# Performance work log

Hardware: AMD Instinct MI355X
Metric: run time of the kernel (lower is better)

The kernel has to match this reference:

```python
import jax, jax.numpy as jnp
import numpy as np

D_MODEL = 1024
N_HEADS = 16
N_KV = N_HEADS // 2
HEAD_DIM = D_MODEL // N_HEADS
HIDDEN = 4 * D_MODEL
B, T = 4, 2048


def setup_inputs() -> dict:
    key = jax.random.key(0)
    ks = jax.random.split(key, 10)
    s = 0.02
    return {
        "x": jax.random.normal(ks[0], (B, T, D_MODEL), dtype=jnp.float32),
        "g1": jnp.ones((D_MODEL,), jnp.float32),
        "g2": jnp.ones((D_MODEL,), jnp.float32),
        "wq": jax.random.normal(ks[1], (D_MODEL, D_MODEL), jnp.float32) * s,
        "wk": jax.random.normal(ks[2], (D_MODEL, N_KV * HEAD_DIM), jnp.float32) * s,
        "wv": jax.random.normal(ks[3], (D_MODEL, N_KV * HEAD_DIM), jnp.float32) * s,
        "wo": jax.random.normal(ks[4], (D_MODEL, D_MODEL), jnp.float32) * s,
        "w1": jax.random.normal(ks[5], (D_MODEL, HIDDEN), jnp.float32) * s,
        "w2": jax.random.normal(ks[6], (D_MODEL, HIDDEN), jnp.float32) * s,
        "w3": jax.random.normal(ks[7], (HIDDEN, D_MODEL), jnp.float32) * s,
    }


def _rmsnorm(x, g, eps=1e-6):
    return x * jax.lax.rsqrt(jnp.mean(x * x, axis=-1, keepdims=True) + eps) * g


def _rope(q, k):
    # q: [B,H,T,d], k: [B,Hkv,T,d]; half-split rotary as in the torch RoPE
    d = q.shape[-1]
    t = jnp.arange(q.shape[2], dtype=jnp.float32)
    inv_freq = 1.0 / (10000.0 ** (jnp.arange(0, d, 2, dtype=jnp.float32) / d))
    freqs = t[:, None] * inv_freq[None, :]            # [T, d/2]
    cos = jnp.cos(freqs)[None, None, :, :]
    sin = jnp.sin(freqs)[None, None, :, :]

    def rot(x):
        x1, x2 = jnp.split(x, 2, axis=-1)
        return jnp.concatenate([x1 * cos - x2 * sin, x2 * cos + x1 * sin], axis=-1)

    return rot(q), rot(k)


def reference(x, g1, g2, wq, wk, wv, wo, w1, w2, w3):
    Bb, Tt, C = x.shape
    h = _rmsnorm(x, g1)
    q = (h @ wq).reshape(Bb, Tt, N_HEADS, HEAD_DIM).transpose(0, 2, 1, 3)
    k = (h @ wk).reshape(Bb, Tt, N_KV, HEAD_DIM).transpose(0, 2, 1, 3)
    v = (h @ wv).reshape(Bb, Tt, N_KV, HEAD_DIM).transpose(0, 2, 1, 3)
    q, k = _rope(q, k)
    rep = N_HEADS // N_KV
    k = jnp.repeat(k, rep, axis=1)
    v = jnp.repeat(v, rep, axis=1)
    att = jnp.einsum("bhtd,bhsd->bhts", q, k) / np.sqrt(HEAD_DIM)
    causal = jnp.tril(jnp.ones((Tt, Tt), dtype=bool))
    att = jnp.where(causal[None, None], att, -jnp.inf)
    att = jax.nn.softmax(att, axis=-1)
    out = jnp.einsum("bhts,bhsd->bhtd", att, v)
    out = out.transpose(0, 2, 1, 3).reshape(Bb, Tt, C) @ wo
    x = x + out
    h2 = _rmsnorm(x, g2)
    ffn = (jax.nn.silu(h2 @ w1) * (h2 @ w2)) @ w3
    return x + ffn
```

## Files before the change

kernel.cpp:

```cpp
#include <hip/hip_runtime.h>
#include <cstdint>

typedef __attribute__((ext_vector_type(8))) short bfrag;
typedef __attribute__((ext_vector_type(4))) float f4;

typedef __attribute__((address_space(1))) const void* gas_t;
typedef __attribute__((address_space(3))) void* las_t;

__device__ __forceinline__ void gload16(const void* g, void* l) {
  __builtin_amdgcn_global_load_lds((gas_t)g, (las_t)l, 16, 0, 0);
}

__device__ __forceinline__ unsigned short f2bf(float f) {
  union { float f; unsigned u; } v; v.f = f;
  unsigned r = v.u + 0x7fffu + ((v.u >> 16) & 1u);
  return (unsigned short)(r >> 16);
}
__device__ __forceinline__ float bf2f(unsigned short b) {
  union { unsigned u; float f; } v; v.u = ((unsigned)b) << 16;
  return v.f;
}
__device__ __forceinline__ unsigned cvt_pk_bf16(float lo, float hi) {
  unsigned r;
  asm("v_cvt_pk_bf16_f32 %0, %1, %2" : "=v"(r) : "v"(lo), "v"(hi));
  return r;
}

__global__ __launch_bounds__(256) void tconv_k(const float* __restrict__ in,
                                               unsigned short* __restrict__ out,
                                               int R, int C) {
  __shared__ unsigned short t[32][33];
  const int c0 = blockIdx.x * 32, r0 = blockIdx.y * 32;
  const int tid = threadIdx.x;
#pragma unroll
  for (int p = 0; p < 4; p++) {
    int flat = p * 256 + tid;
    int r = flat >> 5, c = flat & 31;
    t[r][c] = f2bf(in[(size_t)(r0 + r) * C + c0 + c]);
  }
  __syncthreads();
#pragma unroll
  for (int p = 0; p < 4; p++) {
    int flat = p * 256 + tid;
    int cc = flat >> 5, rr = flat & 31;
    out[(size_t)(c0 + cc) * R + r0 + rr] = t[rr][cc];
  }
}

__global__ __launch_bounds__(256) void rmsnorm_k(const float* __restrict__ x,
                                                 const float* __restrict__ g,
                                                 unsigned short* __restrict__ out) {
  const int row = blockIdx.x, tid = threadIdx.x;
  const float4 v = ((const float4*)(x + (size_t)row * 1024))[tid];
  float ss = v.x * v.x + v.y * v.y + v.z * v.z + v.w * v.w;
#pragma unroll
  for (int off = 1; off < 64; off <<= 1) ss += __shfl_xor(ss, off);
  __shared__ float red[4];
  if ((tid & 63) == 0) red[tid >> 6] = ss;
  __syncthreads();
  float tot = red[0] + red[1] + red[2] + red[3];
  float sc = rsqrtf(tot * (1.0f / 1024.0f) + 1e-6f);
  const float4 gv = ((const float4*)g)[tid];
  ushort4 o;
  o.x = f2bf(v.x * sc * gv.x);
  o.y = f2bf(v.y * sc * gv.y);
  o.z = f2bf(v.z * sc * gv.z);
  o.w = f2bf(v.w * sc * gv.w);
  ((ushort4*)out)[(size_t)row * 256 + tid] = o;
}

template <int MODE>
__global__ __launch_bounds__(256) void gemm_k(const unsigned short* __restrict__ A,
                                              const unsigned short* __restrict__ Bt,
                                              int M, int N, int K,
                                              void* __restrict__ Cout,
                                              const float* __restrict__ resid) {
  __shared__ unsigned short As[128 * 32];
  __shared__ unsigned short Bs[128 * 32];
  const int tid = threadIdx.x;
  const int wid = tid >> 6, lane = tid & 63;
  const int l15 = lane & 15, l4 = lane >> 4;
  const int brow = blockIdx.x * 128, bcol = blockIdx.y * 128;
  const int wr = (wid >> 1) * 64, wc = (wid & 1) * 64;
  f4 acc[4][4];
#pragma unroll
  for (int m = 0; m < 4; m++)
#pragma unroll
    for (int n = 0; n < 4; n++) acc[m][n] = (f4){0.f, 0.f, 0.f, 0.f};

  for (int k0 = 0; k0 < K; k0 += 32) {
#pragma unroll
    for (int c = 0; c < 2; c++) {
      int base = c * 256 + wid * 64;
      int e = base + lane;
      int row = e >> 2, col = (e & 3) * 8;
      gload16(A + (size_t)(brow + row) * K + k0 + col, &As[base * 8]);
      gload16(Bt + (size_t)(bcol + row) * K + k0 + col, &Bs[base * 8]);
    }
    __syncthreads();
    bfrag a[4], b[4];
#pragma unroll
    for (int m = 0; m < 4; m++) a[m] = *(const bfrag*)&As[(wr + m * 16 + l15) * 32 + l4 * 8];
#pragma unroll
    for (int n = 0; n < 4; n++) b[n] = *(const bfrag*)&Bs[(wc + n * 16 + l15) * 32 + l4 * 8];
#pragma unroll
    for (int m = 0; m < 4; m++)
#pragma unroll
      for (int n = 0; n < 4; n++)
        acc[m][n] = __builtin_amdgcn_mfma_f32_16x16x32_bf16(a[m], b[n], acc[m][n], 0, 0, 0);
    __syncthreads();
  }
#pragma unroll
  for (int m = 0; m < 4; m++)
#pragma unroll
    for (int n = 0; n < 4; n++)
#pragma unroll
      for (int j = 0; j < 4; j++) {
        int r = brow + wr + m * 16 + l4 * 4 + j;
        int col = bcol + wc + n * 16 + l15;
        if (MODE == 0) {
          ((unsigned short*)Cout)[(size_t)r * N + col] = f2bf(acc[m][n][j]);
        } else {
          ((float*)Cout)[(size_t)r * N + col] = acc[m][n][j] + resid[(size_t)r * N + col];
        }
      }
}

__global__ __launch_bounds__(256) void ffn1_k(const unsigned short* __restrict__ A,
                                              const unsigned short* __restrict__ B1t,
                                              const unsigned short* __restrict__ B2t,
                                              unsigned short* __restrict__ G,
                                              int M, int N, int K) {
  __shared__ unsigned short As[128 * 32];
  __shared__ unsigned short B1s[128 * 32];
  __shared__ unsigned short B2s[128 * 32];
  const int tid = threadIdx.x;
  const int wid = tid >> 6, lane = tid & 63;
  const int l15 = lane & 15, l4 = lane >> 4;
  const int brow = blockIdx.x * 128, bcol = blockIdx.y * 128;
  const int wr = (wid >> 1) * 64, wc = (wid & 1) * 64;
  f4 acc1[4][4], acc2[4][4];
#pragma unroll
  for (int m = 0; m < 4; m++)
#pragma unroll
    for (int n = 0; n < 4; n++) {
      acc1[m][n] = (f4){0.f, 0.f, 0.f, 0.f};
      acc2[m][n] = (f4){0.f, 0.f, 0.f, 0.f};
    }

  for (int k0 = 0; k0 < K; k0 += 32) {
#pragma unroll
    for (int c = 0; c < 2; c++) {
      int base = c * 256 + wid * 64;
      int e = base + lane;
      int row = e >> 2, col = (e & 3) * 8;
      gload16(A + (size_t)(brow + row) * K + k0 + col, &As[base * 8]);
      gload16(B1t + (size_t)(bcol + row) * K + k0 + col, &B1s[base * 8]);
      gload16(B2t + (size_t)(bcol + row) * K + k0 + col, &B2s[base * 8]);
    }
    __syncthreads();
    bfrag a[4], b1[4], b2[4];
#pragma unroll
    for (int m = 0; m < 4; m++) a[m] = *(const bfrag*)&As[(wr + m * 16 + l15) * 32 + l4 * 8];
#pragma unroll
    for (int n = 0; n < 4; n++) {
      b1[n] = *(const bfrag*)&B1s[(wc + n * 16 + l15) * 32 + l4 * 8];
      b2[n] = *(const bfrag*)&B2s[(wc + n * 16 + l15) * 32 + l4 * 8];
    }
#pragma unroll
    for (int m = 0; m < 4; m++)
#pragma unroll
      for (int n = 0; n < 4; n++) {
        acc1[m][n] = __builtin_amdgcn_mfma_f32_16x16x32_bf16(a[m], b1[n], acc1[m][n], 0, 0, 0);
        acc2[m][n] = __builtin_amdgcn_mfma_f32_16x16x32_bf16(a[m], b2[n], acc2[m][n], 0, 0, 0);
      }
    __syncthreads();
  }
#pragma unroll
  for (int m = 0; m < 4; m++)
#pragma unroll
    for (int n = 0; n < 4; n++)
#pragma unroll
      for (int j = 0; j < 4; j++) {
        int r = brow + wr + m * 16 + l4 * 4 + j;
        int col = bcol + wc + n * 16 + l15;
        float v1 = acc1[m][n][j], v2 = acc2[m][n][j];
        float sg = v1 / (1.0f + expf(-v1));
        G[(size_t)r * N + col] = f2bf(sg * v2);
      }
}

__global__ __launch_bounds__(256) void rope_k(unsigned short* __restrict__ qkv) {
  int idx = blockIdx.x * 256 + threadIdx.x;
  int i = idx & 31;
  int rest = idx >> 5;
  int head = rest % 24;
  int row = rest / 24;
  int t = row & 2047;
  int col = (head < 16) ? (head * 64 + i) : (1024 + (head - 16) * 64 + i);
  size_t base = (size_t)row * 2048 + col;
  float ang = (float)t * exp2f(-(float)i * (13.287712379549449f / 32.0f));
  float s, c;
  sincosf(ang, &s, &c);
  float a = bf2f(qkv[base]), b = bf2f(qkv[base + 32]);
  qkv[base] = f2bf(a * c - b * s);
  qkv[base + 32] = f2bf(b * c + a * s);
}

__global__ __launch_bounds__(256) void vtrans_k(const unsigned short* __restrict__ qkv,
                                                unsigned short* __restrict__ vt) {
  __shared__ unsigned short t[64][65];
  const int t0 = blockIdx.x * 64;
  const int bkh = blockIdx.y;
  const int b = bkh >> 3, kh = bkh & 7;
  const int tid = threadIdx.x;
#pragma unroll
  for (int p = 0; p < 16; p++) {
    int flat = p * 256 + tid;
    int tl = flat >> 6, dl = flat & 63;
    t[tl][dl] = qkv[(size_t)(b * 2048 + t0 + tl) * 2048 + 1536 + kh * 64 + dl];
  }
  __syncthreads();
#pragma unroll
  for (int p = 0; p < 16; p++) {
    int flat = p * 256 + tid;
    int dl = flat >> 6, tl = flat & 63;
    vt[((size_t)(b * 8 + kh) * 64 + dl) * 2048 + t0 + tl] = t[tl][dl];
  }
}

__global__ __launch_bounds__(256) void attn_k(const unsigned short* __restrict__ qkv,
                                              const unsigned short* __restrict__ vt,
                                              unsigned short* __restrict__ out) {
  const int blk = blockIdx.x;
  const int bkh = blk & 31;
  const int tile = 63 - (blk >> 5);
  const int b = bkh >> 3, kh = bkh & 7;
  const int tid = threadIdx.x;
  const int w = tid >> 6, lane = tid & 63, l15 = lane & 15, l4 = lane >> 4;
  const int h = kh * 2 + (w >> 1);
  const int t0w = tile * 32 + (w & 1) * 16;
  const int thi = tile * 32 + 31;

  __shared__ unsigned short KT[2][4096];
  __shared__ unsigned short VT[2][4096];
  __shared__ unsigned short P[4][16 * 72];
  unsigned short* Pw = &P[w][0];

  const unsigned short* qbase = qkv + (size_t)(b * 2048 + t0w + l15) * 2048 + h * 64;
  bfrag q0 = *(const bfrag*)(qbase + l4 * 8);
  bfrag q1 = *(const bfrag*)(qbase + 32 + l4 * 8);

  float mrun = -1e30f, lsum = 0.f;
  f4 o[4];
#pragma unroll
  for (int d = 0; d < 4; d++) o[d] = (f4){0.f, 0.f, 0.f, 0.f};

  const unsigned short* vbase = vt + (size_t)(b * 8 + kh) * 64 * 2048;
  const float sc2 = 0.125f * 1.4426950408889634f;

  auto STAGE = [&](int buf, int s0) {
#pragma unroll
    for (int p = 0; p < 2; ++p) {
      int c = p * 256 + w * 64 + lane;
      int r = c >> 3, sl = (c & 7) ^ (r & 7);
      gload16(qkv + (size_t)(b * 2048 + s0 + r) * 2048 + 1024 + kh * 64 + sl * 8,
              &KT[buf][(p * 256 + w * 64) * 8]);
      gload16(vbase + (size_t)r * 2048 + s0 + sl * 8,
              &VT[buf][(p * 256 + w * 64) * 8]);
    }
  };

  STAGE(0, 0);
  int cur = 0;
  for (int s0 = 0; s0 <= thi; s0 += 64) {
    if (s0 + 64 <= thi) {
      STAGE(cur ^ 1, s0 + 64);
      asm volatile("s_waitcnt vmcnt(4)" ::: "memory");
    } else {
      asm volatile("s_waitcnt vmcnt(0)" ::: "memory");
    }
    __builtin_amdgcn_s_barrier();

    f4 sa[4];
#pragma unroll
    for (int sub = 0; sub < 4; ++sub) {
      int rb = sub * 16 + l15;
      int x = rb & 7;
      bfrag k0 = *(const bfrag*)&KT[cur][(rb * 8 + (l4 ^ x)) * 8];
      bfrag k1 = *(const bfrag*)&KT[cur][(rb * 8 + ((l4 + 4) ^ x)) * 8];
      f4 z = (f4){0.f, 0.f, 0.f, 0.f};
      z = __builtin_amdgcn_mfma_f32_16x16x32_bf16(k0, q0, z, 0, 0, 0);
      z = __builtin_amdgcn_mfma_f32_16x16x32_bf16(k1, q1, z, 0, 0, 0);
      sa[sub] = z;
    }
    const int t = t0w + l15;
    float pv[4][4];
    float mloc = -1e30f;
#pragma unroll
    for (int sub = 0; sub < 4; ++sub)
#pragma unroll
      for (int j = 0; j < 4; ++j) {
        int s = s0 + sub * 16 + l4 * 4 + j;
        float v = sa[sub][j] * sc2;
        if (s > t) v = -1e30f;
        pv[sub][j] = v;
        mloc = fmaxf(mloc, v);
      }
    mloc = fmaxf(mloc, __shfl_xor(mloc, 16));
    mloc = fmaxf(mloc, __shfl_xor(mloc, 32));
    float mnew = fmaxf(mrun, mloc);
    float al = __builtin_amdgcn_exp2f(mrun - mnew);
    mrun = mnew;
    float rs = 0.f;
#pragma unroll
    for (int sub = 0; sub < 4; ++sub)
#pragma unroll
      for (int j = 0; j < 4; ++j) {
        float e = __builtin_amdgcn_exp2f(pv[sub][j] - mnew);
        pv[sub][j] = e;
        rs += e;
      }
    rs += __shfl_xor(rs, 16);
    rs += __shfl_xor(rs, 32);
    lsum = lsum * al + rs;
#pragma unroll
    for (int d = 0; d < 4; d++)
#pragma unroll
      for (int j = 0; j < 4; j++) o[d][j] *= al;

#pragma unroll
    for (int sub = 0; sub < 4; ++sub) {
      uint2 u;
      u.x = cvt_pk_bf16(pv[sub][0], pv[sub][1]);
      u.y = cvt_pk_bf16(pv[sub][2], pv[sub][3]);
      *(uint2*)&Pw[l15 * 72 + sub * 16 + l4 * 4] = u;
    }
#pragma unroll
    for (int sh = 0; sh < 2; ++sh) {
      bfrag pf = *(const bfrag*)&Pw[l15 * 72 + sh * 32 + l4 * 8];
#pragma unroll
      for (int dblk = 0; dblk < 4; ++dblk) {
        int d = dblk * 16 + l15;
        bfrag vf = *(const bfrag*)&VT[cur][(d * 8 + ((sh * 4 + l4) ^ (d & 7))) * 8];
        o[dblk] = __builtin_amdgcn_mfma_f32_16x16x32_bf16(vf, pf, o[dblk], 0, 0, 0);
      }
    }
    asm volatile("s_waitcnt lgkmcnt(0)" ::: "memory");
    __builtin_amdgcn_s_barrier();
    cur ^= 1;
  }
  float inv = 1.0f / lsum;
#pragma unroll
  for (int d = 0; d < 4; d++) {
    ushort4 st;
    st.x = f2bf(o[d][0] * inv);
    st.y = f2bf(o[d][1] * inv);
    st.z = f2bf(o[d][2] * inv);
    st.w = f2bf(o[d][3] * inv);
    *(ushort4*)&out[(size_t)(b * 2048 + t0w + l15) * 1024 + h * 64 + d * 16 + l4 * 4] = st;
  }
}

extern "C" void kernel_launch(void* const* d_in, const int* in_sizes, int n_in,
                              void* d_out, int out_size, void* d_ws, size_t ws_size,
                              hipStream_t stream) {
  const float* x = (const float*)d_in[0];
  const float* g1 = (const float*)d_in[1];
  const float* g2 = (const float*)d_in[2];
  const float* wq = (const float*)d_in[3];
  const float* wk = (const float*)d_in[4];
  const float* wv = (const float*)d_in[5];
  const float* wo = (const float*)d_in[6];
  const float* w1 = (const float*)d_in[7];
  const float* w2 = (const float*)d_in[8];
  const float* w3 = (const float*)d_in[9];

  const size_t MB = 1024 * 1024;
  uint8_t* ws = (uint8_t*)d_ws;
  unsigned short* wqkv_t = (unsigned short*)(ws);
  unsigned short* wo_t = (unsigned short*)(ws + 4 * MB);
  unsigned short* w1_t = (unsigned short*)(ws + 6 * MB);
  unsigned short* w2_t = (unsigned short*)(ws + 14 * MB);
  unsigned short* w3_t = (unsigned short*)(ws + 22 * MB);
  unsigned short* hbuf = (unsigned short*)(ws + 30 * MB);
  unsigned short* qkv = (unsigned short*)(ws + 46 * MB);
  unsigned short* vt = (unsigned short*)(ws + 78 * MB);
  unsigned short* attn_o = (unsigned short*)(ws + 86 * MB);
  unsigned short* gbuf = (unsigned short*)(ws + 46 * MB);
  float* x1 = (float*)(ws + 110 * MB);

  tconv_k<<<dim3(32, 32), 256, 0, stream>>>(wq, wqkv_t, 1024, 1024);
  tconv_k<<<dim3(16, 32), 256, 0, stream>>>(wk, wqkv_t + (size_t)1024 * 1024, 1024, 512);
  tconv_k<<<dim3(16, 32), 256, 0, stream>>>(wv, wqkv_t + (size_t)1536 * 1024, 1024, 512);
  tconv_k<<<dim3(32, 32), 256, 0, stream>>>(wo, wo_t, 1024, 1024);
  tconv_k<<<dim3(128, 32), 256, 0, stream>>>(w1, w1_t, 1024, 4096);
  tconv_k<<<dim3(128, 32), 256, 0, stream>>>(w2, w2_t, 1024, 4096);
  tconv_k<<<dim3(32, 128), 256, 0, stream>>>(w3, w3_t, 4096, 1024);

  rmsnorm_k<<<8192, 256, 0, stream>>>(x, g1, hbuf);
  gemm_k<0><<<dim3(64, 16), 256, 0, stream>>>(hbuf, wqkv_t, 8192, 2048, 1024, qkv, nullptr);
  rope_k<<<24576, 256, 0, stream>>>(qkv);
  vtrans_k<<<dim3(32, 32), 256, 0, stream>>>(qkv, vt);
  attn_k<<<2048, 256, 0, stream>>>(qkv, vt, attn_o);
  gemm_k<1><<<dim3(64, 8), 256, 0, stream>>>(attn_o, wo_t, 8192, 1024, 1024, x1, x);
  rmsnorm_k<<<8192, 256, 0, stream>>>(x1, g2, hbuf);
  ffn1_k<<<dim3(64, 32), 256, 0, stream>>>(hbuf, w1_t, w2_t, gbuf, 8192, 4096, 1024);
  gemm_k<1><<<dim3(64, 8), 256, 0, stream>>>(gbuf, w3_t, 8192, 1024, 4096, (float*)d_out, x1);
}
```

Baseline: 775.7 us.

## Swizzle LDS tiles, remap blocks across XCDs, shrink FFN1 tile

Adds an XOR swizzle to the LDS layout of the GEMM and FFN1 tiles so fragment reads avoid bank conflicts. Remaps block IDs so that consecutive tiles land on the same XCD, which should improve L2 reuse. The FFN1 N-tile is halved to 64 and launch_bounds(256,2) is added, cutting accumulator registers to raise occupancy, at the cost of reloading the A tile twice as often.

```diff
diff --git a/kernel.cpp b/kernel.cpp
--- a/kernel.cpp
+++ b/kernel.cpp
@@ -24,6 +24,15 @@
   unsigned r;
   asm("v_cvt_pk_bf16_f32 %0, %1, %2" : "=v"(r) : "v"(lo), "v"(hi));
   return r;
+}
+
+__device__ __forceinline__ void xcd_swz(int& bx, int& by) {
+  int gx = gridDim.x;
+  int lid = blockIdx.y * gx + blockIdx.x;
+  int nwg = gx * gridDim.y;
+  int swz = (lid & 7) * (nwg >> 3) + (lid >> 3);
+  bx = swz % gx;
+  by = swz / gx;
 }
 
 __global__ __launch_bounds__(256) void tconv_k(const float* __restrict__ in,
@@ -80,8 +89,11 @@
   const int tid = threadIdx.x;
   const int wid = tid >> 6, lane = tid & 63;
   const int l15 = lane & 15, l4 = lane >> 4;
-  const int brow = blockIdx.x * 128, bcol = blockIdx.y * 128;
+  int bx, by;
+  xcd_swz(bx, by);
+  const int brow = bx * 128, bcol = by * 128;
   const int wr = (wid >> 1) * 64, wc = (wid & 1) * 64;
+  const int x15 = l15 & 3;
   f4 acc[4][4];
 #pragma unroll
   for (int m = 0; m < 4; m++)
@@ -91,18 +103,20 @@
   for (int k0 = 0; k0 < K; k0 += 32) {
 #pragma unroll
     for (int c = 0; c < 2; c++) {
-      int base = c * 256 + wid * 64;
-      int e = base + lane;
-      int row = e >> 2, col = (e & 3) * 8;
-      gload16(A + (size_t)(brow + row) * K + k0 + col, &As[base * 8]);
-      gload16(Bt + (size_t)(bcol + row) * K + k0 + col, &Bs[base * 8]);
+      int slot = c * 256 + tid;
+      int r = slot >> 2, cp = slot & 3;
+      int sc = (cp ^ (r & 3)) * 8;
+      gload16(A + (size_t)(brow + r) * K + k0 + sc, &As[slot * 8]);
+      gload16(Bt + (size_t)(bcol + r) * K + k0 + sc, &Bs[slot * 8]);
     }
     __syncthreads();
     bfrag a[4], b[4];
 #pragma unroll
-    for (int m = 0; m < 4; m++) a[m] = *(const bfrag*)&As[(wr + m * 16 + l15) * 32 + l4 * 8];
-#pragma unroll
-    for (int n = 0; n < 4; n++) b[n] = *(const bfrag*)&Bs[(wc + n * 16 + l15) * 32 + l4 * 8];
+    for (int m = 0; m < 4; m++)
+      a[m] = *(const bfrag*)&As[(wr + m * 16 + l15) * 32 + (l4 ^ x15) * 8];
+#pragma unroll
+    for (int n = 0; n < 4; n++)
+      b[n] = *(const bfrag*)&Bs[(wc + n * 16 + l15) * 32 + (l4 ^ x15) * 8];
 #pragma unroll
     for (int m = 0; m < 4; m++)
 #pragma unroll
@@ -126,51 +140,59 @@
       }
 }
 
-__global__ __launch_bounds__(256) void ffn1_k(const unsigned short* __restrict__ A,
-                                              const unsigned short* __restrict__ B1t,
-                                              const unsigned short* __restrict__ B2t,
-                                              unsigned short* __restrict__ G,
-                                              int M, int N, int K) {
+__global__ __launch_bounds__(256, 2) void ffn1_k(const unsigned short* __restrict__ A,
+                                                 const unsigned short* __restrict__ B1t,
+                                                 const unsigned short* __restrict__ B2t,
+                                                 unsigned short* __restrict__ G,
+                                                 int M, int N, int K) {
   __shared__ unsigned short As[128 * 32];
-  __shared__ unsigned short B1s[128 * 32];
-  __shared__ unsigned short B2s[128 * 32];
+  __shared__ unsigned short B1s[64 * 32];
+  __shared__ unsigned short B2s[64 * 32];
   const int tid = threadIdx.x;
   const int wid = tid >> 6, lane = tid & 63;
   const int l15 = lane & 15, l4 = lane >> 4;
-  const int brow = blockIdx.x * 128, bcol = blockIdx.y * 128;
-  const int wr = (wid >> 1) * 64, wc = (wid & 1) * 64;
-  f4 acc1[4][4], acc2[4][4];
+  int bx, by;
+  xcd_swz(bx, by);
+  const int brow = bx * 128, bcol = by * 64;
+  const int wr = (wid >> 1) * 64, wc = (wid & 1) * 32;
+  const int x15 = l15 & 3;
+  f4 acc1[4][2], acc2[4][2];
 #pragma unroll
   for (int m = 0; m < 4; m++)
 #pragma unroll
-    for (int n = 0; n < 4; n++) {
+    for (int n = 0; n < 2; n++) {
       acc1[m][n] = (f4){0.f, 0.f, 0.f, 0.f};
       acc2[m][n] = (f4){0.f, 0.f, 0.f, 0.f};
     }
 
   for (int k0 = 0; k0 < K; k0 += 32) {
 #pragma unroll
-    for (int c = 0; c < 2; c++) {
-      int base = c * 256 + wid * 64;
-      int e = base + lane;
-      int row = e >> 2, col = (e & 3) * 8;
-      gload16(A + (size_t)(brow + row) * K + k0 + col, &As[base * 8]);
-      gload16(B1t + (size_t)(bcol + row) * K + k0 + col, &B1s[base * 8]);
-      gload16(B2t + (size_t)(bcol + row) * K + k0 + col, &B2s[base * 8]);
+    for (int p = 0; p < 2; p++) {
+      int slot = p * 256 + tid;
+      int r = slot >> 2, cp = slot & 3;
+      int sc = (cp ^ (r & 3)) * 8;
+      gload16(A + (size_t)(brow + r) * K + k0 + sc, &As[slot * 8]);
+    }
+    {
+      int r = tid >> 2, cp = tid & 3;
+      int sc = (cp ^ (r & 3)) * 8;
+      gload16(B1t + (size_t)(bcol + r) * K + k0 + sc, &B1s[tid * 8]);
+      gload16(B2t + (size_t)(bcol + r) * K + k0 + sc, &B2s[tid * 8]);
     }
     __syncthreads();
-    bfrag a[4], b1[4], b2[4];
-#pragma unroll
-    for (int m = 0; m < 4; m++) a[m] = *(const bfrag*)&As[(wr + m * 16 + l15) * 32 + l4 * 8];
-#pragma unroll
-    for (int n = 0; n < 4; n++) {
-      b1[n] = *(const bfrag*)&B1s[(wc + n * 16 + l15) * 32 + l4 * 8];
-      b2[n] = *(const bfrag*)&B2s[(wc + n * 16 + l15) * 32 + l4 * 8];
-    }
+    bfrag a[4], b1[2], b2[2];
 #pragma unroll
     for (int m = 0; m < 4; m++)
-#pragma unroll
-      for (int n = 0; n < 4; n++) {
+      a[m] = *(const bfrag*)&As[(wr + m * 16 + l15) * 32 + (l4 ^ x15) * 8];
+#pragma unroll
+    for (int n = 0; n < 2; n++) {
+      b1[n] = *(const bfrag*)&B1s[(wc + n * 16 + l15) * 32 + (l4 ^ x15) * 8];
+      b2[n] = *(const bfrag*)&B2s[(wc + n * 16 + l15) * 32 + (l4 ^ x15) * 8];
+    }
+#pragma unroll
+    for (int m = 0; m < 4; m++)
+#pragma unroll
+      for (int n = 0; n < 2; n++) {
         acc1[m][n] = __builtin_amdgcn_mfma_f32_16x16x32_bf16(a[m], b1[n], acc1[m][n], 0, 0, 0);
         acc2[m][n] = __builtin_amdgcn_mfma_f32_16x16x32_bf16(a[m], b2[n], acc2[m][n], 0, 0, 0);
       }
@@ -179,7 +201,7 @@
 #pragma unroll
   for (int m = 0; m < 4; m++)
 #pragma unroll
-    for (int n = 0; n < 4; n++)
+    for (int n = 0; n < 2; n++)
 #pragma unroll
       for (int j = 0; j < 4; j++) {
         int r = brow + wr + m * 16 + l4 * 4 + j;
@@ -405,6 +427,6 @@
   attn_k<<<2048, 256, 0, stream>>>(qkv, vt, attn_o);
   gemm_k<1><<<dim3(64, 8), 256, 0, stream>>>(attn_o, wo_t, 8192, 1024, 1024, x1, x);
   rmsnorm_k<<<8192, 256, 0, stream>>>(x1, g2, hbuf);
-  ffn1_k<<<dim3(64, 32), 256, 0, stream>>>(hbuf, w1_t, w2_t, gbuf, 8192, 4096, 1024);
+  ffn1_k<<<dim3(64, 64), 256, 0, stream>>>(hbuf, w1_t, w2_t, gbuf, 8192, 4096, 1024);
   gemm_k<1><<<dim3(64, 8), 256, 0, stream>>>(gbuf, w3_t, 8192, 1024, 4096, (float*)d_out, x1);
 }
```

Result: faster. 648.5 us (-16.4%).
